# Kernel optimization log

Measured on AMD Instinct MI355X. Metric: run time of the kernel, lower is better.

The kernel has to match this reference:

```python
import jax, jax.numpy as jnp
import numpy as np

B, IN_C, H, W = 64, 64, 32, 32
OUT_C, KH, KW = 64, 3, 3
STRIDE, PAD, DIL = 1, 1, 1
OUT_H = (H + 2 * PAD - DIL * (KH - 1) - 1) // STRIDE + 1  # 32
OUT_W = (W + 2 * PAD - DIL * (KW - 1) - 1) // STRIDE + 1  # 32


def setup_inputs() -> dict:
    key = jax.random.key(0)
    kx, kw, kb = jax.random.split(key, 3)
    x = jax.random.normal(kx, (B, IN_C, H, W), dtype=jnp.float32)
    n = IN_C * KH * KW
    stdv = 1.0 / np.sqrt(n)
    weight = jax.random.uniform(kw, (OUT_H, OUT_W, OUT_C, IN_C, KH, KW),
                                dtype=jnp.float32, minval=-stdv, maxval=stdv)
    bias = jax.random.uniform(kb, (OUT_C, OUT_H, OUT_W),
                              dtype=jnp.float32, minval=-stdv, maxval=stdv)
    return {"x": x, "weight": weight, "bias": bias}


def _im2col(x):
    # x: [B, C, H, W] -> cols: [B, C*KH*KW, OUT_H*OUT_W], torch.unfold channel-major order
    xp = jnp.pad(x, ((0, 0), (0, 0), (PAD, PAD), (PAD, PAD)))
    patches = []
    for kh in range(KH):
        for kw in range(KW):
            h0, w0 = kh * DIL, kw * DIL
            patches.append(xp[:, :,
                              h0:h0 + (OUT_H - 1) * STRIDE + 1:STRIDE,
                              w0:w0 + (OUT_W - 1) * STRIDE + 1:STRIDE])
    cols = jnp.stack(patches, axis=2)  # [B, C, KH*KW, OUT_H, OUT_W]
    return cols.reshape(x.shape[0], x.shape[1] * KH * KW, OUT_H * OUT_W)


def reference(x, weight, bias):
    cols = _im2col(x)  # [B, K, L] with K = inC*kH*kW, L = outH*outW
    w = weight.reshape(OUT_H * OUT_W, OUT_C, IN_C * KH * KW)  # [L, outC, K]
    # per-location matmul: out[b, l, o] = sum_k cols[b, k, l] * w[l, o, k]
    out = jnp.einsum('bkl,lok->blo', cols, w)
    out = out.reshape(x.shape[0], OUT_H, OUT_W, OUT_C).transpose(0, 3, 1, 2)
    return out + bias[None]
```

## Files before the change

### kernel.cpp

```cpp
#include <hip/hip_runtime.h>
#include <hip/hip_bf16.h>

typedef __attribute__((ext_vector_type(8))) short short8;
typedef __attribute__((ext_vector_type(4))) float f32x4;

__device__ __forceinline__ unsigned short f2bf(float f) {
    union { float f; unsigned int u; } v; v.f = f;
    unsigned int u = v.u;
    u = (u + 0x7FFFu + ((u >> 16) & 1u)) >> 16;
    return (unsigned short)u;
}

__device__ __forceinline__ short8 cvt8(const f32x4 a, const f32x4 b) {
    union { __hip_bfloat162 h[4]; short8 s; } r;
    r.h[0] = __float22bfloat162_rn(make_float2(a[0], a[1]));
    r.h[1] = __float22bfloat162_rn(make_float2(a[2], a[3]));
    r.h[2] = __float22bfloat162_rn(make_float2(b[0], b[1]));
    r.h[3] = __float22bfloat162_rn(make_float2(b[2], b[3]));
    return r.s;
}

__global__ __launch_bounds__(256) void k_xt(const float* __restrict__ x,
                                            unsigned short* __restrict__ xt) {
    const int h  = blockIdx.x;
    const int cg = blockIdx.y;
    const int bh = blockIdx.z;
    const int t  = threadIdx.x;
    __shared__ unsigned short L[32 * 264];

    #pragma unroll
    for (int i = 0; i < 8; ++i) {
        int s   = t + i * 256;
        int row = s >> 3;
        int wq  = s & 7;
        int b = row >> 3, c = row & 7;
        const f32x4 v = *(const f32x4*)(x + (((size_t)((bh * 32 + b) * 64 + cg * 8 + c) * 32 + h) * 32 + wq * 4));
        int base = c * 32 + b;
        L[(wq * 4 + 0) * 264 + base] = f2bf(v[0]);
        L[(wq * 4 + 1) * 264 + base] = f2bf(v[1]);
        L[(wq * 4 + 2) * 264 + base] = f2bf(v[2]);
        L[(wq * 4 + 3) * 264 + base] = f2bf(v[3]);
    }
    __syncthreads();
    #pragma unroll
    for (int i = 0; i < 4; ++i) {
        int s  = t + i * 256;
        int w  = s >> 5;
        int ch = s & 31;
        int c = ch >> 2, b8 = ch & 3;
        short8 v = *(const short8*)&L[w * 264 + c * 32 + b8 * 8];
        *(short8*)(xt + (((size_t)(h * 32 + w) * 64 + cg * 8 + c) * 64 + bh * 32 + b8 * 8)) = v;
    }
}

__global__ __launch_bounds__(256, 4) void k_main(const float* __restrict__ wgt,
                                                 const unsigned short* __restrict__ xt,
                                                 const float* __restrict__ bias,
                                                 unsigned short* __restrict__ ws2b) {
    const int bid = blockIdx.x;
    const int l   = (bid & 7) * 128 + (bid >> 3);
    const int oh = l >> 5, ow = l & 31;
    const int t  = threadIdx.x;
    const int wave = t >> 6, lane = t & 63;
    const int wm = wave >> 1, wn = wave & 1;

    __shared__ unsigned short Ash[2][64 * 72];
    __shared__ unsigned short Bsh[2][64 * 72];

    f32x4 acc[2][2];
    #pragma unroll
    for (int i = 0; i < 2; ++i)
        #pragma unroll
        for (int j = 0; j < 2; ++j)
            acc[i][j] = (f32x4){0.f, 0.f, 0.f, 0.f};

    const int b0 = wave * 16;
    const int o  = t >> 2, kp = t & 3;
    const float* bbase = wgt + (size_t)l * 36864 + o * 576 + kp * 16;

    auto loadA = [&](int kt, short8& va, short8& vb) {
        int kk = kt * 64 + lane;
        int c  = kk / 9;
        int r  = kk - c * 9;
        int kh = r / 3;
        int kw = r - kh * 3;
        int hh = oh + kh - 1;
        int ww = ow + kw - 1;
        va = (short8){0,0,0,0,0,0,0,0};
        vb = (short8){0,0,0,0,0,0,0,0};
        if ((unsigned)hh < 32u && (unsigned)ww < 32u) {
            const unsigned short* src = xt + (((size_t)(hh * 32 + ww) * 64 + c) * 64 + b0);
            va = *(const short8*)src;
            vb = *(const short8*)(src + 8);
        }
    };
    auto loadB = [&](int kt, f32x4 (&bf)[4]) {
        const f32x4* bp = (const f32x4*)(bbase + kt * 64);
        bf[0] = bp[0]; bf[1] = bp[1]; bf[2] = bp[2]; bf[3] = bp[3];
    };

    short8 cA0, cA1;
    short8 nA0 = (short8){0,0,0,0,0,0,0,0}, nA1 = nA0;
    f32x4 bf[4];
    short8 bq0, bq1;

    loadA(0, cA0, cA1);
    loadB(0, bf);
    bq0 = cvt8(bf[0], bf[1]);
    bq1 = cvt8(bf[2], bf[3]);

    for (int kt = 0; kt < 9; ++kt) {
        const int p = kt & 1;
        if (kt < 8) {
            loadA(kt + 1, nA0, nA1);
            loadB(kt + 1, bf);
        }
        #pragma unroll
        for (int j = 0; j < 8; ++j) Ash[p][(b0 + j) * 72 + lane] = (unsigned short)cA0[j];
        #pragma unroll
        for (int j = 0; j < 8; ++j) Ash[p][(b0 + 8 + j) * 72 + lane] = (unsigned short)cA1[j];
        {
            unsigned short* bdst = &Bsh[p][o * 72 + kp * 16];
            *(short8*)bdst       = bq0;
            *(short8*)(bdst + 8) = bq1;
        }
        asm volatile("s_waitcnt lgkmcnt(0)" ::: "memory");
        __builtin_amdgcn_s_barrier();
        __builtin_amdgcn_sched_barrier(0);
        #pragma unroll
        for (int ks = 0; ks < 2; ++ks) {
            int kof = ks * 32 + (lane >> 4) * 8;
            short8 a0 = *(const short8*)&Ash[p][(wm * 32 + (lane & 15)) * 72 + kof];
            short8 a1 = *(const short8*)&Ash[p][(wm * 32 + 16 + (lane & 15)) * 72 + kof];
            short8 q0 = *(const short8*)&Bsh[p][(wn * 32 + (lane & 15)) * 72 + kof];
            short8 q1 = *(const short8*)&Bsh[p][(wn * 32 + 16 + (lane & 15)) * 72 + kof];
            acc[0][0] = __builtin_amdgcn_mfma_f32_16x16x32_bf16(a0, q0, acc[0][0], 0, 0, 0);
            acc[0][1] = __builtin_amdgcn_mfma_f32_16x16x32_bf16(a0, q1, acc[0][1], 0, 0, 0);
            acc[1][0] = __builtin_amdgcn_mfma_f32_16x16x32_bf16(a1, q0, acc[1][0], 0, 0, 0);
            acc[1][1] = __builtin_amdgcn_mfma_f32_16x16x32_bf16(a1, q1, acc[1][1], 0, 0, 0);
        }
        cA0 = nA0; cA1 = nA1;
        if (kt < 8) {
            bq0 = cvt8(bf[0], bf[1]);
            bq1 = cvt8(bf[2], bf[3]);
        }
    }

    const int col = lane & 15;
    const int rq  = (lane >> 4) * 4;
    #pragma unroll
    for (int j = 0; j < 2; ++j) {
        int n = wn * 32 + j * 16 + col;
        float bv = bias[n * 1024 + l];
        #pragma unroll
        for (int i = 0; i < 2; ++i) {
            int mbase = wm * 32 + i * 16 + rq;
            #pragma unroll
            for (int q = 0; q < 4; ++q) {
                ws2b[(size_t)l * 4096 + (size_t)(mbase + q) * 64 + n] = f2bf(acc[i][j][q] + bv);
            }
        }
    }
}

__global__ __launch_bounds__(256) void k_out(const unsigned short* __restrict__ ws2b,
                                             float* __restrict__ out) {
    const int bx = blockIdx.x;
    const int lt = bx & 15;
    const int mt = bx >> 4;
    const int t  = threadIdx.x;
    __shared__ float T[64 * 65];
    const int l0 = lt * 64, m0 = mt * 64;

    #pragma unroll
    for (int i = 0; i < 2; ++i) {
        int s  = t + i * 256;
        int lr = s >> 3;
        int mc = (s & 7) * 8;
        short8 v = *(const short8*)&ws2b[(size_t)(l0 + lr) * 4096 + m0 + mc];
        #pragma unroll
        for (int j = 0; j < 8; ++j) {
            union { unsigned int u; float f; } w;
            w.u = ((unsigned int)(unsigned short)v[j]) << 16;
            T[lr * 65 + mc + j] = w.f;
        }
    }
    __syncthreads();
    #pragma unroll
    for (int i = 0; i < 4; ++i) {
        int s  = t + i * 256;
        int mr = s >> 4;
        int lc = (s & 15) * 4;
        f32x4 v;
        v[0] = T[(lc + 0) * 65 + mr];
        v[1] = T[(lc + 1) * 65 + mr];
        v[2] = T[(lc + 2) * 65 + mr];
        v[3] = T[(lc + 3) * 65 + mr];
        *(f32x4*)(out + (size_t)(m0 + mr) * 1024 + l0 + lc) = v;
    }
}

__global__ __launch_bounds__(256) void k_naive(const float* __restrict__ x,
                                               const float* __restrict__ wgt,
                                               const float* __restrict__ bias,
                                               float* __restrict__ out) {
    int idx = blockIdx.x * 256 + threadIdx.x;
    int ow = idx & 31, oh = (idx >> 5) & 31, o = (idx >> 10) & 63, b = idx >> 16;
    float acc = bias[(o * 32 + oh) * 32 + ow];
    const float* wp = wgt + ((size_t)(oh * 32 + ow) * 64 + o) * 576;
    for (int c = 0; c < 64; ++c) {
        for (int kh = 0; kh < 3; ++kh) {
            int hh = oh + kh - 1;
            if ((unsigned)hh >= 32u) continue;
            for (int kw = 0; kw < 3; ++kw) {
                int ww = ow + kw - 1;
                if ((unsigned)ww >= 32u) continue;
                acc += x[((size_t)(b * 64 + c) * 32 + hh) * 32 + ww] * wp[c * 9 + kh * 3 + kw];
            }
        }
    }
    out[idx] = acc;
}

extern "C" void kernel_launch(void* const* d_in, const int* in_sizes, int n_in,
                              void* d_out, int out_size, void* d_ws, size_t ws_size,
                              hipStream_t stream) {
    const float* x    = (const float*)d_in[0];
    const float* wgt  = (const float*)d_in[1];
    const float* bias = (const float*)d_in[2];
    float* out = (float*)d_out;

    const size_t xt_bytes  = (size_t)32 * 32 * 64 * 64 * 2;
    const size_t ws2_bytes = (size_t)1024 * 4096 * 2;

    if (ws_size >= xt_bytes + ws2_bytes) {
        unsigned short* xt   = (unsigned short*)d_ws;
        unsigned short* ws2b = (unsigned short*)((char*)d_ws + xt_bytes);
        k_xt<<<dim3(32, 8, 2), 256, 0, stream>>>(x, xt);
        k_main<<<1024, 256, 0, stream>>>(wgt, xt, bias, ws2b);
        k_out<<<1024, 256, 0, stream>>>(ws2b, out);
    } else {
        k_naive<<<(64 * 64 * 32 * 32) / 256, 256, 0, stream>>>(x, wgt, bias, out);
    }
}
```

Baseline: 44.99 us.

## Prefetch two k-steps ahead in main loop and split transpose kernel finer

The main GEMM loop now keeps two stages of A and B register prefetch in flight instead of one, and the loop is fully unrolled so the double-indexed register arrays can stay in registers. This is meant to hide more global-load latency behind the MFMA work. Separately, the input transpose/convert kernel handles 16 batches per block instead of 32, doubling its grid and halving its shared memory. The cost is higher register pressure in k_main, which could cut occupancy under the 4-blocks-per-CU launch bound.

```diff
diff --git a/kernel.cpp b/kernel.cpp
--- a/kernel.cpp
+++ b/kernel.cpp
@@ -24,32 +24,32 @@
                                             unsigned short* __restrict__ xt) {
     const int h  = blockIdx.x;
     const int cg = blockIdx.y;
-    const int bh = blockIdx.z;
+    const int bq = blockIdx.z;
     const int t  = threadIdx.x;
-    __shared__ unsigned short L[32 * 264];
-
-    #pragma unroll
-    for (int i = 0; i < 8; ++i) {
+    __shared__ unsigned short L[32 * 136];
+
+    #pragma unroll
+    for (int i = 0; i < 4; ++i) {
         int s   = t + i * 256;
         int row = s >> 3;
         int wq  = s & 7;
         int b = row >> 3, c = row & 7;
-        const f32x4 v = *(const f32x4*)(x + (((size_t)((bh * 32 + b) * 64 + cg * 8 + c) * 32 + h) * 32 + wq * 4));
-        int base = c * 32 + b;
-        L[(wq * 4 + 0) * 264 + base] = f2bf(v[0]);
-        L[(wq * 4 + 1) * 264 + base] = f2bf(v[1]);
-        L[(wq * 4 + 2) * 264 + base] = f2bf(v[2]);
-        L[(wq * 4 + 3) * 264 + base] = f2bf(v[3]);
+        const f32x4 v = *(const f32x4*)(x + (((size_t)((bq * 16 + b) * 64 + cg * 8 + c) * 32 + h) * 32 + wq * 4));
+        int base = c * 16 + b;
+        L[(wq * 4 + 0) * 136 + base] = f2bf(v[0]);
+        L[(wq * 4 + 1) * 136 + base] = f2bf(v[1]);
+        L[(wq * 4 + 2) * 136 + base] = f2bf(v[2]);
+        L[(wq * 4 + 3) * 136 + base] = f2bf(v[3]);
     }
     __syncthreads();
     #pragma unroll
-    for (int i = 0; i < 4; ++i) {
+    for (int i = 0; i < 2; ++i) {
         int s  = t + i * 256;
-        int w  = s >> 5;
-        int ch = s & 31;
-        int c = ch >> 2, b8 = ch & 3;
-        short8 v = *(const short8*)&L[w * 264 + c * 32 + b8 * 8];
-        *(short8*)(xt + (((size_t)(h * 32 + w) * 64 + cg * 8 + c) * 64 + bh * 32 + b8 * 8)) = v;
+        int w  = s >> 4;
+        int c  = (s >> 1) & 7;
+        int b8 = s & 1;
+        short8 v = *(const short8*)&L[w * 136 + c * 16 + b8 * 8];
+        *(short8*)(xt + (((size_t)(h * 32 + w) * 64 + cg * 8 + c) * 64 + bq * 16 + b8 * 8)) = v;
     }
 }
 
@@ -99,26 +99,26 @@
         bf[0] = bp[0]; bf[1] = bp[1]; bf[2] = bp[2]; bf[3] = bp[3];
     };
 
-    short8 cA0, cA1;
-    short8 nA0 = (short8){0,0,0,0,0,0,0,0}, nA1 = nA0;
-    f32x4 bf[4];
+    short8 pA0[2], pA1[2];
+    f32x4 bf[2][4];
     short8 bq0, bq1;
 
-    loadA(0, cA0, cA1);
-    loadB(0, bf);
-    bq0 = cvt8(bf[0], bf[1]);
-    bq1 = cvt8(bf[2], bf[3]);
-
+    loadA(0, pA0[0], pA1[0]);
+    loadB(0, bf[0]);
+    loadA(1, pA0[1], pA1[1]);
+    loadB(1, bf[1]);
+    bq0 = cvt8(bf[0][0], bf[0][1]);
+    bq1 = cvt8(bf[0][2], bf[0][3]);
+
+    #pragma unroll
     for (int kt = 0; kt < 9; ++kt) {
         const int p = kt & 1;
-        if (kt < 8) {
-            loadA(kt + 1, nA0, nA1);
-            loadB(kt + 1, bf);
-        }
-        #pragma unroll
-        for (int j = 0; j < 8; ++j) Ash[p][(b0 + j) * 72 + lane] = (unsigned short)cA0[j];
-        #pragma unroll
-        for (int j = 0; j < 8; ++j) Ash[p][(b0 + 8 + j) * 72 + lane] = (unsigned short)cA1[j];
+        if (kt + 2 < 9) loadB(kt + 2, bf[p]);
+        #pragma unroll
+        for (int j = 0; j < 8; ++j) Ash[p][(b0 + j) * 72 + lane] = (unsigned short)pA0[p][j];
+        #pragma unroll
+        for (int j = 0; j < 8; ++j) Ash[p][(b0 + 8 + j) * 72 + lane] = (unsigned short)pA1[p][j];
+        if (kt + 2 < 9) loadA(kt + 2, pA0[p], pA1[p]);
         {
             unsigned short* bdst = &Bsh[p][o * 72 + kp * 16];
             *(short8*)bdst       = bq0;
@@ -139,10 +139,9 @@
             acc[1][0] = __builtin_amdgcn_mfma_f32_16x16x32_bf16(a1, q0, acc[1][0], 0, 0, 0);
             acc[1][1] = __builtin_amdgcn_mfma_f32_16x16x32_bf16(a1, q1, acc[1][1], 0, 0, 0);
         }
-        cA0 = nA0; cA1 = nA1;
-        if (kt < 8) {
-            bq0 = cvt8(bf[0], bf[1]);
-            bq1 = cvt8(bf[2], bf[3]);
+        if (kt + 1 < 9) {
+            bq0 = cvt8(bf[(kt + 1) & 1][0], bf[(kt + 1) & 1][1]);
+            bq1 = cvt8(bf[(kt + 1) & 1][2], bf[(kt + 1) & 1][3]);
         }
     }
 
@@ -236,7 +235,7 @@
     if (ws_size >= xt_bytes + ws2_bytes) {
         unsigned short* xt   = (unsigned short*)d_ws;
         unsigned short* ws2b = (unsigned short*)((char*)d_ws + xt_bytes);
-        k_xt<<<dim3(32, 8, 2), 256, 0, stream>>>(x, xt);
+        k_xt<<<dim3(32, 8, 4), 256, 0, stream>>>(x, xt);
         k_main<<<1024, 256, 0, stream>>>(wgt, xt, bias, ws2b);
         k_out<<<1024, 256, 0, stream>>>(ws2b, out);
     } else {
```

Measured after the change: 44.42 us (median of 2 runs). Within noise of the previous version (-1.3%).
